# Performance work log

Hardware: AMD Instinct MI355X
Metric: run time of the kernel (lower is better)

Reference implementation:

```python
import jax, jax.numpy as jnp
import numpy as np
import math

PHI = (1.0 + math.sqrt(5.0)) / 2.0
ALPHA = 0.01
I_ROT = math.pi / 2.0
B, IN, H = 4096, 1024, 1024
GIN = IN + 4 * H  # input + 2H (h flat) + 2H (surfaced flat)


def _mag(z):
    return jnp.sqrt(z[..., 0] ** 2 + z[..., 1] ** 2 + 1e-8)


def _phase(z):
    return jnp.arctan2(z[..., 1], z[..., 0] + 1e-10)


@jax.custom_vjp
def fractal_compress(mag):
    m = jnp.maximum(mag, 1e-8)
    return m ** (2.0 / 3.0)


def _fc_fwd(mag):
    m = jnp.maximum(mag, 1e-8)
    c = m ** (2.0 / 3.0)
    return c, c / (m + 1e-6)


def _fc_bwd(ratio, g):
    return (g * jnp.minimum(ratio, 2.0),)


fractal_compress.defvjp(_fc_fwd, _fc_bwd)


def converge(z):
    mag = _mag(z)
    ph = _phase(z)
    cm = fractal_compress(mag)
    return jnp.stack([cm * jnp.cos(ph), cm * jnp.sin(ph)], axis=-1)


def resonance_gate(a, b):
    d = _phase(a) - _phase(b)
    return jnp.cos(d / 2.0) ** 2


def _uni(k, shape, fan_in):
    s = (1.0 / PHI) / math.sqrt(fan_in)
    return jax.random.uniform(k, shape, jnp.float32, -s, s)


def setup_inputs() -> dict:
    key = jax.random.key(0)
    ks = jax.random.split(key, 12)
    return {
        "x_t": jax.random.normal(ks[0], (B, IN), jnp.float32),
        "h_prev": jax.random.normal(ks[1], (B, H, 2), jnp.float32),
        "c_prev": jax.random.normal(ks[2], (B, H, 2), jnp.float32),
        "d_prev": jax.random.normal(ks[3], (B, H, 2), jnp.float32),
        "b_prev": jax.random.uniform(ks[4], (B, 1), jnp.float32),
        "Wf_w": _uni(ks[5], (H, GIN), GIN), "Wf_b": jnp.zeros((H,), jnp.float32),
        "Wi_w": _uni(ks[6], (H, GIN), GIN), "Wi_b": jnp.zeros((H,), jnp.float32),
        "Wo_w": _uni(ks[7], (H, GIN), GIN), "Wo_b": jnp.zeros((H,), jnp.float32),
        "Wc_w": _uni(ks[8], (2 * H, GIN), GIN), "Wc_b": jnp.zeros((2 * H,), jnp.float32),
        "Wr_w": _uni(ks[9], (2 * H, IN), IN), "Wr_b": jnp.zeros((2 * H,), jnp.float32),
        "theta": jnp.full((H,), I_ROT, jnp.float32),
    }


def reference(x_t, h_prev, c_prev, d_prev, b_prev,
              Wf_w, Wf_b, Wi_w, Wi_b, Wo_w, Wo_b, Wc_w, Wc_b, Wr_w, Wr_b, theta):
    batch = x_t.shape[0]
    hid = theta.shape[0]

    # boundary: real input -> complex
    x_complex = (x_t @ Wr_w.T + Wr_b).reshape(batch, hid, 2)

    # memory surfacing from the (detached) worldline
    d_read = jax.lax.stop_gradient(d_prev)
    T = resonance_gate(x_complex, d_read)                      # (B, H)
    d_mag = _mag(d_read)[..., None]                            # (B, H, 1)
    d_normed = d_read / (d_mag + 1e-8)
    d_scale = jnp.sqrt(jnp.clip(d_mag, 1e-6, 20.0))
    surfaced = d_normed * d_scale * T[..., None]               # (B, H, 2)

    combined = jnp.concatenate(
        [x_t, h_prev.reshape(batch, -1), surfaced.reshape(batch, -1)], axis=-1)

    f_raw = combined @ Wf_w.T + Wf_b
    i_raw = combined @ Wi_w.T + Wi_b
    o_raw = combined @ Wo_w.T + Wo_b

    temperature = (2.0 * b_prev + 1e-4)[..., None]             # (B, 1, 1)
    gate_stack = jnp.stack([f_raw, i_raw, o_raw], axis=-1)     # (B, H, 3)
    gw = jax.nn.softmax(gate_stack / temperature, axis=-1)
    f_t, i_t, o_t = gw[..., 0], gw[..., 1], gw[..., 2]

    g_raw = combined @ Wc_w.T + Wc_b
    g_t = jnp.stack([jnp.tanh(g_raw[:, :hid]), jnp.tanh(g_raw[:, hid:])], axis=-1)

    # convergence: released surface -> fractal-compressed -> worldline
    released = (1.0 - f_t)[..., None] * c_prev
    compressed = jnp.clip(converge(released), -10.0, 10.0)
    d_t = jax.lax.stop_gradient(d_prev) + ALPHA * compressed
    d_mag_new = _mag(d_t)[..., None]
    d_t = jnp.where(d_mag_new > 20.0, d_t * (20.0 / d_mag_new), d_t)

    # cell update + i-rotation
    c_updated = f_t[..., None] * c_prev + i_t[..., None] * g_t
    cos_t = jnp.cos(theta)[None, :, None]
    sin_t = jnp.sin(theta)[None, :, None]
    cr, ci = c_updated[..., 0:1], c_updated[..., 1:2]
    c_t = jnp.concatenate([cos_t * cr - sin_t * ci, sin_t * cr + cos_t * ci], axis=-1)

    c_squashed = jnp.stack([jnp.tanh(c_t[..., 0]), jnp.tanh(c_t[..., 1])], axis=-1)
    h_raw = o_t[..., None] * c_squashed
    G = resonance_gate(h_raw, d_t)
    h_t = G[..., None] * h_raw

    # balance update from energy split
    conv_e = (_mag(released) ** 2).sum(axis=-1, keepdims=True)
    emer_e = (_mag(h_t) ** 2).sum(axis=-1, keepdims=True)
    b_measured = conv_e / (conv_e + emer_e + 1e-8)
    b_t = 0.99 * b_prev + 0.01 * b_measured

    h_t = jnp.nan_to_num(h_t, nan=0.0)
    c_t = jnp.nan_to_num(c_t, nan=0.0)
    d_t = jnp.nan_to_num(d_t, nan=0.0)
    b_t = jnp.nan_to_num(b_t, nan=0.5)
    return (h_t, c_t, d_t, b_t)
```

## Files before the change

### kernel.cpp

```cpp
#include <hip/hip_runtime.h>
#include <math.h>

typedef unsigned short u16;
typedef unsigned int u32;
typedef u16 u16x4 __attribute__((ext_vector_type(4)));
typedef float f32x2 __attribute__((ext_vector_type(2)));
typedef float f32x4 __attribute__((ext_vector_type(4)));
typedef __bf16 bf16x8 __attribute__((ext_vector_type(8)));

__device__ __forceinline__ u16 f2bf(float f){
  u32 u = __builtin_bit_cast(u32, f);
  u32 r = u + 0x7FFFu + ((u >> 16) & 1u);
  return (u16)(r >> 16);
}
__device__ __forceinline__ float bf2f(u16 h){
  u32 u = ((u32)h) << 16;
  return __builtin_bit_cast(float, u);
}
__device__ __forceinline__ float ftanh(float x){
  float e = __expf(2.f*x);
  return 1.f - 2.f/(e+1.f);
}

typedef __attribute__((address_space(1))) const unsigned int gas_u32;
typedef __attribute__((address_space(3))) unsigned int las_u32;
__device__ __forceinline__ void gload_lds16(const void* g, void* l){
  __builtin_amdgcn_global_load_lds((gas_u32*)g, (las_u32*)l, 16, 0, 0);
}

__global__ __launch_bounds__(256) void cvt_hi(const float* __restrict__ in, u16* __restrict__ out, int n4){
  int i = blockIdx.x*256 + threadIdx.x;
  if (i >= n4) return;
  f32x4 v = *(const f32x4*)(in + (size_t)i*4);
  u16x4 o;
  #pragma unroll
  for (int j=0;j<4;++j) o[j]=f2bf(v[j]);
  *(u16x4*)(out + (size_t)i*4) = o;
}

__global__ __launch_bounds__(256) void cvt_hilo(const float* __restrict__ in, u16* __restrict__ hi, u16* __restrict__ lo, int n4){
  int i = blockIdx.x*256 + threadIdx.x;
  if (i >= n4) return;
  f32x4 v = *(const f32x4*)(in + (size_t)i*4);
  u16x4 oh, ol;
  #pragma unroll
  for (int j=0;j<4;++j){ u16 h=f2bf(v[j]); oh[j]=h; ol[j]=f2bf(v[j]-bf2f(h)); }
  *(u16x4*)(hi + (size_t)i*4) = oh;
  *(u16x4*)(lo + (size_t)i*4) = ol;
}

__global__ __launch_bounds__(256) void cvt_xh(const float* __restrict__ x, const float* __restrict__ h,
                                              u16* __restrict__ cA, u16* __restrict__ xlo){
  int b = blockIdx.y;
  int c0 = (blockIdx.x*256 + threadIdx.x)*4;
  f32x4 v;
  if (c0 < 1024) v = *(const f32x4*)(x + (size_t)b*1024 + c0);
  else           v = *(const f32x4*)(h + (size_t)b*2048 + (c0-1024));
  u16x4 hi4;
  #pragma unroll
  for (int j=0;j<4;++j) hi4[j]=f2bf(v[j]);
  *(u16x4*)(cA + (size_t)b*5120 + c0) = hi4;
  if (c0 < 1024){
    u16x4 lo4;
    #pragma unroll
    for (int j=0;j<4;++j) lo4[j]=f2bf(v[j]-bf2f(hi4[j]));
    *(u16x4*)(xlo + (size_t)b*1024 + c0) = lo4;
  }
}

__global__ __launch_bounds__(256) void prep_surf(const float* __restrict__ xc, const float* __restrict__ dp,
                                                 const int* __restrict__ smap, float* __restrict__ Scmp,
                                                 u16* __restrict__ cA, int cap){
  int i = blockIdx.x*256 + threadIdx.x;
  int b = i >> 10, h = i & 1023;
  f32x2 z = *(const f32x2*)(xc + 2*(size_t)i);
  f32x2 d = *(const f32x2*)(dp + 2*(size_t)i);
  float zx = z[0] + 1e-10f, dx = d[0] + 1e-10f;
  float hz = sqrtf(zx*zx + z[1]*z[1]);
  float hd = sqrtf(dx*dx + d[1]*d[1]);
  float cosd = (zx*dx + z[1]*d[1]) / fmaxf(hz*hd, 1e-30f);
  float T = 0.5f + 0.5f*cosd;
  float dmag = sqrtf(d[0]*d[0] + d[1]*d[1] + 1e-8f);
  float dscale = sqrtf(fminf(fmaxf(dmag, 1e-6f), 20.0f));
  float s = T * dscale / (dmag + 1e-8f);
  float o0 = d[0]*s, o1 = d[1]*s;
  u32 pk = (u32)f2bf(o0) | ((u32)f2bf(o1) << 16);
  *(u32*)&cA[(size_t)b*5120 + 3072 + 2*h] = pk;
  int p = smap[b];
  if (p >= 0 && p < cap)
    *(f32x2*)(Scmp + ((size_t)p*1024 + h)*2) = f32x2{o0, o1};
}

__global__ __launch_bounds__(256) void flag_rows(const float* __restrict__ bp, int* __restrict__ out,
                                                 int* __restrict__ smap, int cap){
  __shared__ int cnt;
  if (threadIdx.x==0) cnt=0;
  __syncthreads();
  for (int i=threadIdx.x; i<4096; i+=256){
    int p = -1;
    if (bp[i] < 0.04f){
      p = atomicAdd(&cnt,1);
      if (p < cap) out[1+p]=i;
    }
    smap[i] = p;
  }
  __syncthreads();
  if (threadIdx.x==0) out[0] = min(cnt, cap);
}

__global__ __launch_bounds__(256) void fix_init(const int* __restrict__ smap, const int* __restrict__ cr,
    const float* __restrict__ b0, const float* __restrict__ b1, const float* __restrict__ b2,
    float* __restrict__ C){
  int b = blockIdx.x;
  int p = smap[b];
  if (p < 0 || p >= cr[0]) return;
  #pragma unroll
  for (int j0=0; j0<3072; j0+=256){
    int j = j0 + threadIdx.x;
    float bb = (j<1024) ? b0[j] : ((j<2048) ? b1[j-1024] : b2[j-2048]);
    C[(size_t)b*3072 + j] = bb;
  }
}

#define LDA8(BUF,H,MH,J) (*(const bf16x8*)(sAc + ((BUF)*2+(H))*16384 + abase + (MH)*4096 + (J)*1024))
#define LDB8(BUF,H,N)    (*(const bf16x8*)(sBc + ((BUF)*2+(H))*BHTB + bbase + (N)*1024))
#define STG_A8(BUF,H,TT) { const u16* s_ = Ah + aS + (size_t)(TT)*64 + (H)*32; \
    gload_lds16(s_, dA + ((BUF)*2+(H))*8192); \
    gload_lds16(s_ + aS2, dA + ((BUF)*2+(H))*8192 + 4096); }
#define STG_B8(BUF,H,TT) { const u16* s_ = Bh + bS + (size_t)(TT)*64 + (H)*32; \
    gload_lds16(s_, dB + ((BUF)*2+(H))*(BHTB/2)); \
    if constexpr (NR==4){ gload_lds16(s_ + bS2, dB + ((BUF)*2+(H))*(BHTB/2) + 4096); } }
#define PH8(BUF,H,MH,RB,STG,DOW) do{ \
    bf16x8 af0 = LDA8(BUF,H,MH,0), af1 = LDA8(BUF,H,MH,1), af2 = LDA8(BUF,H,MH,2), af3 = LDA8(BUF,H,MH,3); \
    if (RB){ _Pragma("unroll") for(int n_=0;n_<NR;++n_) bfr[n_] = LDB8(BUF,H,n_); } \
    STG; \
    asm volatile("" ::: "memory"); \
    __builtin_amdgcn_s_barrier(); \
    asm volatile("s_waitcnt lgkmcnt(0)" ::: "memory"); \
    __builtin_amdgcn_sched_barrier(0); \
    __builtin_amdgcn_s_setprio(1); \
    _Pragma("unroll") for(int n_=0;n_<NR;++n_){ \
      acc[(MH)*4+0][n_] = __builtin_amdgcn_mfma_f32_16x16x32_bf16(af0, bfr[n_], acc[(MH)*4+0][n_],0,0,0); \
      acc[(MH)*4+1][n_] = __builtin_amdgcn_mfma_f32_16x16x32_bf16(af1, bfr[n_], acc[(MH)*4+1][n_],0,0,0); \
      acc[(MH)*4+2][n_] = __builtin_amdgcn_mfma_f32_16x16x32_bf16(af2, bfr[n_], acc[(MH)*4+2][n_],0,0,0); \
      acc[(MH)*4+3][n_] = __builtin_amdgcn_mfma_f32_16x16x32_bf16(af3, bfr[n_], acc[(MH)*4+3][n_],0,0,0); } \
    __builtin_amdgcn_s_setprio(0); \
    if (DOW) { asm volatile("s_waitcnt vmcnt(%0)" :: "i"(VN) : "memory"); } \
    asm volatile("" ::: "memory"); \
    __builtin_amdgcn_s_barrier(); \
    __builtin_amdgcn_sched_barrier(0); \
  }while(0)

template<int NR, bool OUTBF, int NB>
__global__ __launch_bounds__(512) void gemm8p(
    const u16* __restrict__ Ah, int lda,
    const u16* __restrict__ Bh, int ldb,
    const float* __restrict__ bias0, const float* __restrict__ bias1, const float* __restrict__ bias2,
    float* __restrict__ Cf, u16* __restrict__ Cb, int ldc, int K)
{
  constexpr int BN   = NR*64;
  constexpr int BHTB = BN*64;
  constexpr int VN   = (NR==4) ? 4 : 3;
  __shared__ u16 sA[4*8192];
  __shared__ u16 sB[4*(NR*2048)];
  const char* sAc = (const char*)sA;
  const char* sBc = (const char*)sB;

  const int tid = threadIdx.x, lane = tid&63, w8 = tid>>6;
  const int wr = w8>>2, wc = w8&3;
  const int l16 = lane&15;

  const int gx = gridDim.x, nwg = gx*gridDim.y;
  const int lin = blockIdx.y*gx + blockIdx.x;
  const int sw = (lin&7)*(nwg>>3) + (lin>>3);
  const int m0 = (sw / gx)*256, n0 = (sw % gx)*BN;

  const int rowS  = tid>>2;
  const int ksS   = (tid&3) ^ ((tid>>3)&3);
  const size_t aS = (size_t)(m0 + rowS)*lda + ksS*8;
  const size_t aS2= (size_t)128*lda;
  const size_t bS = (size_t)(n0 + rowS)*ldb + ksS*8;
  const size_t bS2= (size_t)128*ldb;
  u16* dA = sA + w8*512;
  u16* dB = sB + w8*512;

  const int aslot = (lane>>4) ^ ((l16>>1)&3);
  const int abase = (wr*128 + l16)*64 + aslot*16;
  const int bbase = (wc*(NR*16) + l16)*64 + aslot*16;

  f32x4 acc[8][NR];
  #pragma unroll
  for (int a=0;a<8;++a)
    #pragma unroll
    for (int b=0;b<NR;++b) acc[a][b] = f32x4{0.f,0.f,0.f,0.f};
  bf16x8 bfr[NR];

  const int NT = K>>6, NITER = K>>7;

  STG_A8(0,0,0) STG_B8(0,0,0) STG_A8(0,1,0) STG_B8(0,1,0) STG_A8(1,0,1) STG_B8(1,0,1)
  asm volatile("s_waitcnt vmcnt(%0)" :: "i"(VN) : "memory");
  asm volatile("" ::: "memory");
  __builtin_amdgcn_s_barrier();
  __builtin_amdgcn_sched_barrier(0);

  for (int i=0; i<NITER; ++i){
    const int t1 = 2*i+1;
    const int ta = min(2*i+2, NT-1);
    const int tb = min(2*i+3, NT-1);
    PH8(0,0,0,true,  STG_A8(1,1,t1), false);
    PH8(0,0,1,false, STG_B8(1,1,t1), false);
    PH8(0,1,0,true,  STG_A8(0,0,ta), false);
    PH8(0,1,1,false, STG_B8(0,0,ta), true);
    PH8(1,0,0,true,  STG_A8(0,1,ta), false);
    PH8(1,0,1,false, STG_B8(0,1,ta), false);
    PH8(1,1,0,true,  STG_A8(1,0,tb), false);
    PH8(1,1,1,false, STG_B8(1,0,tb), true);
  }
  asm volatile("s_waitcnt vmcnt(0)" ::: "memory");

  #pragma unroll
  for (int mf=0; mf<8; ++mf){
    int grow = m0 + wr*128 + mf*16 + (lane>>4)*4;
    #pragma unroll
    for (int n=0; n<NR; ++n){
      int gcol = n0 + wc*(NR*16) + n*16 + l16;
      float bb;
      if constexpr(NB==3) bb = (gcol<1024) ? bias0[gcol] : ((gcol<2048) ? bias1[gcol-1024] : bias2[gcol-2048]);
      else bb = bias0[gcol];
      #pragma unroll
      for (int r2=0;r2<4;++r2){
        float v = acc[mf][n][r2] + bb;
        if constexpr(OUTBF) Cb[(size_t)(grow+r2)*ldc + gcol] = f2bf(v);
        else                Cf[(size_t)(grow+r2)*ldc + gcol] = v;
      }
    }
  }
}

#define STG128(USRC, BW) do{ int u_=(USRC)<NT?(USRC):NT-1; \
    { const u16* s_=Ah+aS+(size_t)u_*32; gload_lds16(s_, sA+(BW)*4096+ldsb); } \
    { const u16* s_=Bh+bS+(size_t)u_*32; gload_lds16(s_, sB+(BW)*8192+ldsb); \
      gload_lds16(s_+bS2, sB+(BW)*8192+4096+ldsb); } \
    if constexpr(SPLIT){ \
      const u16* s2_=Al+aSl+(size_t)u_*32; gload_lds16(s2_, sAl+(BW)*4096+ldsb); \
      const u16* s3_=Bl+bS+(size_t)u_*32;  gload_lds16(s3_, sBl+(BW)*8192+ldsb); \
      gload_lds16(s3_+bS2, sBl+(BW)*8192+4096+ldsb); } \
  }while(0)

template<bool SPLIT, bool OUTBF>
__global__ __launch_bounds__(512) void gemm128(
    const u16* __restrict__ Ah, int lda,
    const u16* __restrict__ Al, int ldal,
    const u16* __restrict__ Bh, int ldb,
    const u16* __restrict__ Bl,
    const float* __restrict__ bias0,
    float* __restrict__ Cf, u16* __restrict__ Cb, int ldc, int K)
{
  constexpr int VN = SPLIT ? 6 : 3;
  __shared__ u16 sA [3*4096];
  __shared__ u16 sB [3*8192];
  __shared__ u16 sAl[SPLIT?3*4096:8];
  __shared__ u16 sBl[SPLIT?3*8192:8];

  const int tid=threadIdx.x, lane=tid&63, w8=tid>>6;
  const int wr=w8>>2, wc=w8&3, l16=lane&15;

  const int gx=gridDim.x, nwg=gx*gridDim.y;
  const int lin=blockIdx.y*gx+blockIdx.x;
  const int sw=(lin&7)*(nwg>>3)+(lin>>3);
  const int m0=(sw/gx)*128, n0=(sw%gx)*256;

  const int rowS=tid>>2;
  const int ksS=(tid&3)^((tid>>3)&3);
  const size_t aS =(size_t)(m0+rowS)*lda  + ksS*8;
  const size_t aSl=(size_t)(m0+rowS)*(size_t)ldal + ksS*8;
  const size_t bS =(size_t)(n0+rowS)*ldb  + ksS*8;
  const size_t bS2=(size_t)128*ldb;
  const int ldsb = w8*512;

  const int aslot=(lane>>4)^((l16>>1)&3);
  const int abase=(wr*64+l16)*64 + aslot*16;
  const int bbase=(wc*64+l16)*64 + aslot*16;

  f32x4 acc[4][4];
  #pragma unroll
  for (int a=0;a<4;++a)
    #pragma unroll
    for (int b=0;b<4;++b) acc[a][b] = f32x4{0.f,0.f,0.f,0.f};

  const int NT = K>>5;

  STG128(0,0); STG128(1,1);
  asm volatile("s_waitcnt vmcnt(%0)" :: "i"(VN) : "memory");
  asm volatile("" ::: "memory");
  __builtin_amdgcn_s_barrier();
  __builtin_amdgcn_sched_barrier(0);

  int bufR = 0;
  for (int t=0; t<NT; ++t){
    int bufW = bufR+2; if (bufW>=3) bufW-=3;
    const char* sAc=(const char*)sA  + bufR*8192;
    const char* sBc=(const char*)sB  + bufR*16384;
    const char* sAlc=(const char*)sAl + bufR*8192;
    const char* sBlc=(const char*)sBl + bufR*16384;
    bf16x8 af[4], bf[4], afl[4], bfl[4];
    #pragma unroll
    for (int f=0; f<4; ++f){
      af[f] = *(const bf16x8*)(sAc + abase + f*1024);
      bf[f] = *(const bf16x8*)(sBc + bbase + f*1024);
      if constexpr(SPLIT){
        afl[f] = *(const bf16x8*)(sAlc + abase + f*1024);
        bfl[f] = *(const bf16x8*)(sBlc + bbase + f*1024);
      }
    }
    STG128(t+2, bufW);
    asm volatile("" ::: "memory");
    __builtin_amdgcn_s_barrier();
    asm volatile("s_waitcnt lgkmcnt(0)" ::: "memory");
    __builtin_amdgcn_sched_barrier(0);
    __builtin_amdgcn_s_setprio(1);
    #pragma unroll
    for (int mf=0; mf<4; ++mf){
      #pragma unroll
      for (int nf=0; nf<4; ++nf){
        acc[mf][nf] = __builtin_amdgcn_mfma_f32_16x16x32_bf16(af[mf], bf[nf], acc[mf][nf],0,0,0);
        if constexpr(SPLIT){
          acc[mf][nf] = __builtin_amdgcn_mfma_f32_16x16x32_bf16(afl[mf], bf[nf],  acc[mf][nf],0,0,0);
          acc[mf][nf] = __builtin_amdgcn_mfma_f32_16x16x32_bf16(af[mf],  bfl[nf], acc[mf][nf],0,0,0);
        }
      }
    }
    __builtin_amdgcn_s_setprio(0);
    asm volatile("s_waitcnt vmcnt(%0)" :: "i"(VN) : "memory");
    asm volatile("" ::: "memory");
    __builtin_amdgcn_s_barrier();
    __builtin_amdgcn_sched_barrier(0);
    bufR = (bufR==2) ? 0 : bufR+1;
  }
  asm volatile("s_waitcnt vmcnt(0)" ::: "memory");

  #pragma unroll
  for (int mf=0; mf<4; ++mf){
    int grow = m0 + wr*64 + mf*16 + (lane>>4)*4;
    #pragma unroll
    for (int nf=0; nf<4; ++nf){
      int gcol = n0 + wc*64 + nf*16 + l16;
      float bb = bias0[gcol];
      #pragma unroll
      for (int r2=0;r2<4;++r2){
        float v = acc[mf][nf][r2] + bb;
        if constexpr(OUTBF) Cb[(size_t)(grow+r2)*ldc + gcol] = f2bf(v);
        else                Cf[(size_t)(grow+r2)*ldc + gcol] = v;
      }
    }
  }
}

#define LSTR 40
#define FIX_KC 16
#define FIX_KLEN 320
__global__ __launch_bounds__(256) void gemm_fix_sk(
    const float* __restrict__ Xs, const float* __restrict__ Hs,
    const float* __restrict__ Scmp, const int* __restrict__ smap,
    const float* __restrict__ W0, const float* __restrict__ W1, const float* __restrict__ W2,
    const int* __restrict__ cr, float* __restrict__ C)
{
  const int count = cr[0];
  const int m0 = blockIdx.y * 128;
  if (m0 >= count) return;
  const int* rows = cr + 1;
  const int kbeg = blockIdx.z * FIX_KLEN;
  const int kend = kbeg + FIX_KLEN;

  __shared__ u16 sAh[128*LSTR];
  __shared__ u16 sAl[128*LSTR];
  __shared__ u16 sBh[128*LSTR];
  __shared__ u16 sBl[128*LSTR];

  const int tid = threadIdx.x;
  const int n0 = blockIdx.x * 128;
  int seg = n0 >> 10;
  const float* W = (seg==0) ? W0 : (seg==1 ? W1 : W2);
  int nw = n0 & 1023;

  const int wave = tid >> 6, lane = tid & 63;
  const int wm = wave >> 1, wn = wave & 1;
  const int l16 = lane & 15, lk8 = (lane >> 4) * 8;

  f32x4 acc[4][4];
  #pragma unroll
  for (int a=0;a<4;++a)
    #pragma unroll
    for (int b=0;b<4;++b) acc[a][b] = f32x4{0.f,0.f,0.f,0.f};

  for (int k0 = kbeg; k0 < kend; k0 += 32){
    #pragma unroll
    for (int i=0;i<4;++i){
      int flat = tid + i*256;
      int r  = flat >> 3;
      int c4 = flat & 7;
      int kk = k0 + c4*4;
      int mrow = rows[min(m0 + r, count-1)];
      const float* srcA;
      if (kk < 1024)      srcA = Xs + (size_t)mrow*1024 + kk;
      else if (kk < 3072) srcA = Hs + (size_t)mrow*2048 + (kk - 1024);
      else                srcA = Scmp + (size_t)smap[mrow]*2048 + (kk - 3072);
      f32x4 va = *(const f32x4*)srcA;
      f32x4 vb = *(const f32x4*)(W + (size_t)(nw + r)*5120 + kk);
      u16x4 ah, bh, al, bl;
      #pragma unroll
      for (int j=0;j<4;++j){
        u16 hA = f2bf(va[j]); ah[j] = hA; al[j] = f2bf(va[j] - bf2f(hA));
        u16 hB = f2bf(vb[j]); bh[j] = hB; bl[j] = f2bf(vb[j] - bf2f(hB));
      }
      int o = r*LSTR + c4*4;
      *(u16x4*)&sAh[o] = ah;
      *(u16x4*)&sBh[o] = bh;
      *(u16x4*)&sAl[o] = al;
      *(u16x4*)&sBl[o] = bl;
    }
    __syncthreads();
    bf16x8 fah[4], fbh[4], fal[4], fbl[4];
    #pragma unroll
    for (int f=0; f<4; ++f){
      int ra  = (wm*64 + f*16 + l16)*LSTR + lk8;
      int rb2 = (wn*64 + f*16 + l16)*LSTR + lk8;
      fah[f] = *(const bf16x8*)&sAh[ra];
      fbh[f] = *(const bf16x8*)&sBh[rb2];
      fal[f] = *(const bf16x8*)&sAl[ra];
      fbl[f] = *(const bf16x8*)&sBl[rb2];
    }
    #pragma unroll
    for (int fm=0; fm<4; ++fm){
      #pragma unroll
      for (int fn=0; fn<4; ++fn){
        acc[fm][fn] = __builtin_amdgcn_mfma_f32_16x16x32_bf16(fah[fm], fbh[fn], acc[fm][fn], 0,0,0);
        acc[fm][fn] = __builtin_amdgcn_mfma_f32_16x16x32_bf16(fal[fm], fbh[fn], acc[fm][fn], 0,0,0);
        acc[fm][fn] = __builtin_amdgcn_mfma_f32_16x16x32_bf16(fah[fm], fbl[fn], acc[fm][fn], 0,0,0);
      }
    }
    __syncthreads();
  }

  #pragma unroll
  for (int fm=0; fm<4; ++fm){
    int trow = wm*64 + fm*16 + (lane>>4)*4;
    #pragma unroll
    for (int fn=0; fn<4; ++fn){
      int lcol = wn*64 + fn*16 + l16;
      #pragma unroll
      for (int r2=0;r2<4;++r2){
        int mi = m0 + trow + r2;
        if (mi < count){
          int mrow = rows[mi];
          atomicAdd(&C[(size_t)mrow*3072 + (n0 + lcol)], acc[fm][fn][r2]);
        }
      }
    }
  }
}

__global__ __launch_bounds__(256) void epilogue(
    const float* __restrict__ rawfio, const u16* __restrict__ rawg,
    const float* __restrict__ c_prev, const float* __restrict__ d_prev,
    const float* __restrict__ b_prev, const float* __restrict__ theta,
    float* __restrict__ out)
{
  const int b = blockIdx.x;
  const int tid = threadIdx.x;
  float* Hout = out;
  float* Cout = out + (size_t)8388608;
  float* Dout = out + (size_t)16777216;
  float* Bout = out + (size_t)25165824;
  const float bp = b_prev[b];
  const float inv_t = 1.0f / (2.0f*bp + 1e-4f);
  float conv_acc = 0.f, emer_acc = 0.f;
  const size_t rb3 = (size_t)b*3072;
  const size_t rg = (size_t)b*2048;

  #pragma unroll
  for (int j=0;j<4;++j){
    int h = tid + j*256;
    float fr = rawfio[rb3 + h];
    float ir = rawfio[rb3 + 1024 + h];
    float og = rawfio[rb3 + 2048 + h];
    float g0 = bf2f(rawg[rg + h]);
    float g1 = bf2f(rawg[rg + 1024 + h]);

    float mx = fmaxf(fr, fmaxf(ir, og));
    float ef = __expf((fr-mx)*inv_t);
    float ei = __expf((ir-mx)*inv_t);
    float eo = __expf((og-mx)*inv_t);
    float inv_s = 1.0f/(ef+ei+eo);
    float ft = ef*inv_s, it = ei*inv_s, ot = eo*inv_s;

    f32x2 cp = *(const f32x2*)(c_prev + 2*((size_t)b*1024 + h));
    f32x2 dp = *(const f32x2*)(d_prev + 2*((size_t)b*1024 + h));

    float r0 = (1.f-ft)*cp[0], r1 = (1.f-ft)*cp[1];
    float rm2 = r0*r0 + r1*r1;
    conv_acc += rm2 + 1e-8f;
    float rmag = sqrtf(rm2 + 1e-8f);
    float cm = __expf(0.66666667f * __logf(rmag));
    float rx = r0 + 1e-10f;
    float hr = fmaxf(sqrtf(rx*rx + r1*r1), 1e-30f);
    float invhr = cm / hr;
    float comp0 = fminf(fmaxf(rx*invhr, -10.f), 10.f);
    float comp1 = fminf(fmaxf(r1*invhr, -10.f), 10.f);

    float d0 = dp[0] + 0.01f*comp0;
    float d1 = dp[1] + 0.01f*comp1;
    float dmn = sqrtf(d0*d0 + d1*d1 + 1e-8f);
    if (dmn > 20.f){ float sc = 20.f/dmn; d0*=sc; d1*=sc; }

    float gt0 = ftanh(g0), gt1 = ftanh(g1);
    float cu0 = ft*cp[0] + it*gt0;
    float cu1 = ft*cp[1] + it*gt1;
    float th = theta[h];
    float sth, cth;
    __sincosf(th, &sth, &cth);
    float c0 = cth*cu0 - sth*cu1;
    float c1 = sth*cu0 + cth*cu1;
    float cs0 = ftanh(c0), cs1 = ftanh(c1);
    float hr0 = ot*cs0, hr1 = ot*cs1;

    float hx = hr0 + 1e-10f, dx = d0 + 1e-10f;
    float hh = sqrtf(hx*hx + hr1*hr1);
    float hd = sqrtf(dx*dx + d1*d1);
    float cosd = (hx*dx + hr1*d1) / fmaxf(hh*hd, 1e-30f);
    float G = 0.5f + 0.5f*cosd;
    float h0 = G*hr0, h1 = G*hr1;
    emer_acc += h0*h0 + h1*h1 + 1e-8f;

    h0 = (h0==h0)?h0:0.f;  h1 = (h1==h1)?h1:0.f;
    c0 = (c0==c0)?c0:0.f;  c1 = (c1==c1)?c1:0.f;
    d0 = (d0==d0)?d0:0.f;  d1 = (d1==d1)?d1:0.f;

    size_t oi = 2*((size_t)b*1024 + h);
    *(f32x2*)(Hout+oi) = f32x2{h0,h1};
    *(f32x2*)(Cout+oi) = f32x2{c0,c1};
    *(f32x2*)(Dout+oi) = f32x2{d0,d1};
  }

  #pragma unroll
  for (int off=32; off; off>>=1){
    conv_acc += __shfl_down(conv_acc, off);
    emer_acc += __shfl_down(emer_acc, off);
  }
  __shared__ float sred[8];
  int wv = tid>>6, ln = tid&63;
  if (ln==0){ sred[wv]=conv_acc; sred[4+wv]=emer_acc; }
  __syncthreads();
  if (tid==0){
    float cv = sred[0]+sred[1]+sred[2]+sred[3];
    float em = sred[4]+sred[5]+sred[6]+sred[7];
    float bm = cv/(cv+em+1e-8f);
    float bt = 0.99f*bp + 0.01f*bm;
    bt = (bt==bt)?bt:0.5f;
    Bout[b] = bt;
  }
}

extern "C" void kernel_launch(void* const* d_in, const int* in_sizes, int n_in,
                              void* d_out, int out_size, void* d_ws, size_t ws_size,
                              hipStream_t stream)
{
  const float* x_t    = (const float*)d_in[0];
  const float* h_prev = (const float*)d_in[1];
  const float* c_prev = (const float*)d_in[2];
  const float* d_prev = (const float*)d_in[3];
  const float* b_prev = (const float*)d_in[4];
  const float* Wf_w   = (const float*)d_in[5];
  const float* Wf_b   = (const float*)d_in[6];
  const float* Wi_w   = (const float*)d_in[7];
  const float* Wi_b   = (const float*)d_in[8];
  const float* Wo_w   = (const float*)d_in[9];
  const float* Wo_b   = (const float*)d_in[10];
  const float* Wc_w   = (const float*)d_in[11];
  const float* Wc_b   = (const float*)d_in[12];
  const float* Wr_w   = (const float*)d_in[13];
  const float* Wr_b   = (const float*)d_in[14];
  const float* theta  = (const float*)d_in[15];

  char* W = (char*)d_ws;
  float* rawfio = (float*)W;
  float* xc     = (float*)W;
  u16*   Wr_hi  = (u16*)(W + 50331648);
  u16*   Wr_lo  = (u16*)(W + 50331648 + 4194304);
  u16*   x_lo   = (u16*)(W + 50331648 + 8388608);
  u16*   raw_g  = (u16*)(W + 50331648);
  u16*   cA     = (u16*)(W + 67108864);
  u16*   WD     = (u16*)(W + 109051904);
  int*   idx    = (int*)(W + 140509184);
  int*   smap   = (int*)(W + 140509184 + 16388);
  float* Scmp   = (float*)(W + 140546048);
  long long avail = (long long)ws_size - 140546048LL;
  int cap = (int)(avail > 0 ? avail / 8192 : 0);
  if (cap > 1024) cap = 1024;

  dim3 blk(256);

  cvt_xh<<<dim3(3,4096), blk, 0, stream>>>(x_t, h_prev, cA, x_lo);
  cvt_hilo<<<2048, blk, 0, stream>>>(Wr_w, Wr_hi, Wr_lo, 524288);
  gemm128<true,false><<<dim3(8,32), dim3(512), 0, stream>>>(
      cA, 5120, x_lo, 1024, Wr_hi, 1024, Wr_lo,
      Wr_b, xc, nullptr, 2048, 1024);
  flag_rows<<<1, blk, 0, stream>>>(b_prev, idx, smap, cap);
  prep_surf<<<16384, blk, 0, stream>>>(xc, d_prev, smap, Scmp, cA, cap);
  cvt_hi<<<5120, blk, 0, stream>>>(Wf_w, WD, 1310720);
  cvt_hi<<<5120, blk, 0, stream>>>(Wi_w, WD + (size_t)1024*5120, 1310720);
  cvt_hi<<<5120, blk, 0, stream>>>(Wo_w, WD + (size_t)2048*5120, 1310720);
  gemm8p<4,false,3><<<dim3(12,16), dim3(512), 0, stream>>>(
      cA, 5120, WD, 5120, Wf_b, Wi_b, Wo_b, rawfio, nullptr, 3072, 5120);
  fix_init<<<4096, blk, 0, stream>>>(smap, idx, Wf_b, Wi_b, Wo_b, rawfio);
  gemm_fix_sk<<<dim3(24,8,FIX_KC), blk, 0, stream>>>(
      x_t, h_prev, Scmp, smap, Wf_w, Wi_w, Wo_w, idx, rawfio);
  cvt_hi<<<10240, blk, 0, stream>>>(Wc_w, WD, 2621440);
  gemm128<false,true><<<dim3(8,32), dim3(512), 0, stream>>>(
      cA, 5120, nullptr, 0, WD, 5120, nullptr,
      Wc_b, nullptr, raw_g, 2048, 5120);
  epilogue<<<4096, blk, 0, stream>>>(rawfio, raw_g, c_prev, d_prev, b_prev, theta, (float*)d_out);
}
```

Baseline: 525.4 us.

## Fuse prep kernels, decouple fix-up GEMM output, deepen gemm128 pipeline

Merges the x/h conversion, Wr hi/lo split, rawfix zeroing and row flagging into one prep0 launch, and the three weight conversions into one cvtW3 launch. The fix-up GEMM now accumulates into a separate compact rawfix buffer indexed by flagged-row position. The epilogue adds the biases and selects that buffer for flagged rows, which removes fix_init and the ordering dependency on gemm8p. The Wc gemm128 uses five LDS stages instead of three for deeper prefetch, and gemm8p waits on loads more often. This trades more LDS per block (lower occupancy risk) and a fixed cap of 256 flagged rows for fewer launches and better overlap.

```diff
diff --git a/kernel.cpp b/kernel.cpp
--- a/kernel.cpp
+++ b/kernel.cpp
@@ -8,6 +8,8 @@
 typedef float f32x4 __attribute__((ext_vector_type(4)));
 typedef __bf16 bf16x8 __attribute__((ext_vector_type(8)));
 
+#define CAPF 256
+
 __device__ __forceinline__ u16 f2bf(float f){
   u32 u = __builtin_bit_cast(u32, f);
   u32 r = u + 0x7FFFu + ((u >> 16) & 1u);
@@ -26,6 +28,73 @@
 typedef __attribute__((address_space(3))) unsigned int las_u32;
 __device__ __forceinline__ void gload_lds16(const void* g, void* l){
   __builtin_amdgcn_global_load_lds((gas_u32*)g, (las_u32*)l, 16, 0, 0);
+}
+
+__global__ __launch_bounds__(256) void prep0(
+    const float* __restrict__ x, const float* __restrict__ h,
+    u16* __restrict__ cA, u16* __restrict__ xlo,
+    const float* __restrict__ Wr, u16* __restrict__ Wr_hi, u16* __restrict__ Wr_lo,
+    const float* __restrict__ bp, int* __restrict__ idx, int* __restrict__ smap,
+    float* __restrict__ rawfix)
+{
+  const int bx = blockIdx.x, tid = threadIdx.x;
+  if (bx < 12288){
+    int b = bx / 3, cb = bx - b*3;
+    int c0 = (cb*256 + tid)*4;
+    f32x4 v;
+    if (c0 < 1024) v = *(const f32x4*)(x + (size_t)b*1024 + c0);
+    else           v = *(const f32x4*)(h + (size_t)b*2048 + (c0-1024));
+    u16x4 hi4;
+    #pragma unroll
+    for (int j=0;j<4;++j) hi4[j]=f2bf(v[j]);
+    *(u16x4*)(cA + (size_t)b*5120 + c0) = hi4;
+    if (c0 < 1024){
+      u16x4 lo4;
+      #pragma unroll
+      for (int j=0;j<4;++j) lo4[j]=f2bf(v[j]-bf2f(hi4[j]));
+      *(u16x4*)(xlo + (size_t)b*1024 + c0) = lo4;
+    }
+  } else if (bx < 14336){
+    int i = (bx-12288)*256 + tid;
+    f32x4 v = *(const f32x4*)(Wr + (size_t)i*4);
+    u16x4 oh, ol;
+    #pragma unroll
+    for (int j=0;j<4;++j){ u16 hh=f2bf(v[j]); oh[j]=hh; ol[j]=f2bf(v[j]-bf2f(hh)); }
+    *(u16x4*)(Wr_hi + (size_t)i*4) = oh;
+    *(u16x4*)(Wr_lo + (size_t)i*4) = ol;
+  } else if (bx < 15104){
+    int i = (bx-14336)*256 + tid;
+    *(f32x4*)(rawfix + (size_t)i*4) = f32x4{0.f,0.f,0.f,0.f};
+  } else {
+    __shared__ int cnt;
+    if (tid==0) cnt=0;
+    __syncthreads();
+    for (int i=tid; i<4096; i+=256){
+      int p = -1;
+      if (bp[i] < 0.04f){
+        p = atomicAdd(&cnt,1);
+        if (p < CAPF) idx[1+p]=i;
+      }
+      smap[i] = p;
+    }
+    __syncthreads();
+    if (tid==0) idx[0] = min(cnt, CAPF);
+  }
+}
+
+__global__ __launch_bounds__(256) void cvtW3(
+    const float* __restrict__ W0, const float* __restrict__ W1, const float* __restrict__ W2,
+    u16* __restrict__ out)
+{
+  int i = blockIdx.x*256 + threadIdx.x;
+  int seg = i / 1310720;
+  int w = i - seg*1310720;
+  const float* src = (seg==0) ? W0 : (seg==1 ? W1 : W2);
+  f32x4 v = *(const f32x4*)(src + (size_t)w*4);
+  u16x4 o;
+  #pragma unroll
+  for (int j=0;j<4;++j) o[j]=f2bf(v[j]);
+  *(u16x4*)(out + (size_t)seg*5242880 + (size_t)w*4) = o;
 }
 
 __global__ __launch_bounds__(256) void cvt_hi(const float* __restrict__ in, u16* __restrict__ out, int n4){
@@ -38,39 +107,9 @@
   *(u16x4*)(out + (size_t)i*4) = o;
 }
 
-__global__ __launch_bounds__(256) void cvt_hilo(const float* __restrict__ in, u16* __restrict__ hi, u16* __restrict__ lo, int n4){
-  int i = blockIdx.x*256 + threadIdx.x;
-  if (i >= n4) return;
-  f32x4 v = *(const f32x4*)(in + (size_t)i*4);
-  u16x4 oh, ol;
-  #pragma unroll
-  for (int j=0;j<4;++j){ u16 h=f2bf(v[j]); oh[j]=h; ol[j]=f2bf(v[j]-bf2f(h)); }
-  *(u16x4*)(hi + (size_t)i*4) = oh;
-  *(u16x4*)(lo + (size_t)i*4) = ol;
-}
-
-__global__ __launch_bounds__(256) void cvt_xh(const float* __restrict__ x, const float* __restrict__ h,
-                                              u16* __restrict__ cA, u16* __restrict__ xlo){
-  int b = blockIdx.y;
-  int c0 = (blockIdx.x*256 + threadIdx.x)*4;
-  f32x4 v;
-  if (c0 < 1024) v = *(const f32x4*)(x + (size_t)b*1024 + c0);
-  else           v = *(const f32x4*)(h + (size_t)b*2048 + (c0-1024));
-  u16x4 hi4;
-  #pragma unroll
-  for (int j=0;j<4;++j) hi4[j]=f2bf(v[j]);
-  *(u16x4*)(cA + (size_t)b*5120 + c0) = hi4;
-  if (c0 < 1024){
-    u16x4 lo4;
-    #pragma unroll
-    for (int j=0;j<4;++j) lo4[j]=f2bf(v[j]-bf2f(hi4[j]));
-    *(u16x4*)(xlo + (size_t)b*1024 + c0) = lo4;
-  }
-}
-
 __global__ __launch_bounds__(256) void prep_surf(const float* __restrict__ xc, const float* __restrict__ dp,
                                                  const int* __restrict__ smap, float* __restrict__ Scmp,
-                                                 u16* __restrict__ cA, int cap){
+                                                 u16* __restrict__ cA){
   int i = blockIdx.x*256 + threadIdx.x;
   int b = i >> 10, h = i & 1023;
   f32x2 z = *(const f32x2*)(xc + 2*(size_t)i);
@@ -87,39 +126,8 @@
   u32 pk = (u32)f2bf(o0) | ((u32)f2bf(o1) << 16);
   *(u32*)&cA[(size_t)b*5120 + 3072 + 2*h] = pk;
   int p = smap[b];
-  if (p >= 0 && p < cap)
+  if (p >= 0 && p < CAPF)
     *(f32x2*)(Scmp + ((size_t)p*1024 + h)*2) = f32x2{o0, o1};
-}
-
-__global__ __launch_bounds__(256) void flag_rows(const float* __restrict__ bp, int* __restrict__ out,
-                                                 int* __restrict__ smap, int cap){
-  __shared__ int cnt;
-  if (threadIdx.x==0) cnt=0;
-  __syncthreads();
-  for (int i=threadIdx.x; i<4096; i+=256){
-    int p = -1;
-    if (bp[i] < 0.04f){
-      p = atomicAdd(&cnt,1);
-      if (p < cap) out[1+p]=i;
-    }
-    smap[i] = p;
-  }
-  __syncthreads();
-  if (threadIdx.x==0) out[0] = min(cnt, cap);
-}
-
-__global__ __launch_bounds__(256) void fix_init(const int* __restrict__ smap, const int* __restrict__ cr,
-    const float* __restrict__ b0, const float* __restrict__ b1, const float* __restrict__ b2,
-    float* __restrict__ C){
-  int b = blockIdx.x;
-  int p = smap[b];
-  if (p < 0 || p >= cr[0]) return;
-  #pragma unroll
-  for (int j0=0; j0<3072; j0+=256){
-    int j = j0 + threadIdx.x;
-    float bb = (j<1024) ? b0[j] : ((j<2048) ? b1[j-1024] : b2[j-2048]);
-    C[(size_t)b*3072 + j] = bb;
-  }
 }
 
 #define LDA8(BUF,H,MH,J) (*(const bf16x8*)(sAc + ((BUF)*2+(H))*16384 + abase + (MH)*4096 + (J)*1024))
@@ -129,7 +137,7 @@
     gload_lds16(s_ + aS2, dA + ((BUF)*2+(H))*8192 + 4096); }
 #define STG_B8(BUF,H,TT) { const u16* s_ = Bh + bS + (size_t)(TT)*64 + (H)*32; \
     gload_lds16(s_, dB + ((BUF)*2+(H))*(BHTB/2)); \
-    if constexpr (NR==4){ gload_lds16(s_ + bS2, dB + ((BUF)*2+(H))*(BHTB/2) + 4096); } }
+    gload_lds16(s_ + bS2, dB + ((BUF)*2+(H))*(BHTB/2) + 4096); }
 #define PH8(BUF,H,MH,RB,STG,DOW) do{ \
     bf16x8 af0 = LDA8(BUF,H,MH,0), af1 = LDA8(BUF,H,MH,1), af2 = LDA8(BUF,H,MH,2), af3 = LDA8(BUF,H,MH,3); \
     if (RB){ _Pragma("unroll") for(int n_=0;n_<NR;++n_) bfr[n_] = LDB8(BUF,H,n_); } \
@@ -160,7 +168,7 @@
 {
   constexpr int BN   = NR*64;
   constexpr int BHTB = BN*64;
-  constexpr int VN   = (NR==4) ? 4 : 3;
+  constexpr int VN   = 8;
   __shared__ u16 sA[4*8192];
   __shared__ u16 sB[4*(NR*2048)];
   const char* sAc = (const char*)sA;
@@ -208,11 +216,11 @@
     const int ta = min(2*i+2, NT-1);
     const int tb = min(2*i+3, NT-1);
     PH8(0,0,0,true,  STG_A8(1,1,t1), false);
-    PH8(0,0,1,false, STG_B8(1,1,t1), false);
+    PH8(0,0,1,false, STG_B8(1,1,t1), true);
     PH8(0,1,0,true,  STG_A8(0,0,ta), false);
     PH8(0,1,1,false, STG_B8(0,0,ta), true);
     PH8(1,0,0,true,  STG_A8(0,1,ta), false);
-    PH8(1,0,1,false, STG_B8(0,1,ta), false);
+    PH8(1,0,1,false, STG_B8(0,1,ta), true);
     PH8(1,1,0,true,  STG_A8(1,0,tb), false);
     PH8(1,1,1,false, STG_B8(1,0,tb), true);
   }
@@ -247,7 +255,7 @@
       gload_lds16(s3_+bS2, sBl+(BW)*8192+4096+ldsb); } \
   }while(0)
 
-template<bool SPLIT, bool OUTBF>
+template<bool SPLIT, bool OUTBF, int BUFS>
 __global__ __launch_bounds__(512) void gemm128(
     const u16* __restrict__ Ah, int lda,
     const u16* __restrict__ Al, int ldal,
@@ -256,11 +264,13 @@
     const float* __restrict__ bias0,
     float* __restrict__ Cf, u16* __restrict__ Cb, int ldc, int K)
 {
-  constexpr int VN = SPLIT ? 6 : 3;
-  __shared__ u16 sA [3*4096];
-  __shared__ u16 sB [3*8192];
-  __shared__ u16 sAl[SPLIT?3*4096:8];
-  __shared__ u16 sBl[SPLIT?3*8192:8];
+  constexpr int LPS = SPLIT ? 6 : 3;
+  constexpr int VN  = (BUFS-2)*LPS;
+  constexpr int PRE = BUFS-1;
+  __shared__ u16 sA [BUFS*4096];
+  __shared__ u16 sB [BUFS*8192];
+  __shared__ u16 sAl[SPLIT?BUFS*4096:8];
+  __shared__ u16 sBl[SPLIT?BUFS*8192:8];
 
   const int tid=threadIdx.x, lane=tid&63, w8=tid>>6;
   const int wr=w8>>2, wc=w8&3, l16=lane&15;
@@ -290,7 +300,8 @@
 
   const int NT = K>>5;
 
-  STG128(0,0); STG128(1,1);
+  #pragma unroll
+  for (int u=0; u<PRE; ++u){ STG128(u,u); }
   asm volatile("s_waitcnt vmcnt(%0)" :: "i"(VN) : "memory");
   asm volatile("" ::: "memory");
   __builtin_amdgcn_s_barrier();
@@ -298,7 +309,7 @@
 
   int bufR = 0;
   for (int t=0; t<NT; ++t){
-    int bufW = bufR+2; if (bufW>=3) bufW-=3;
+    int bufW = (bufR==0) ? BUFS-1 : bufR-1;
     const char* sAc=(const char*)sA  + bufR*8192;
     const char* sBc=(const char*)sB  + bufR*16384;
     const char* sAlc=(const char*)sAl + bufR*8192;
@@ -313,7 +324,7 @@
         bfl[f] = *(const bf16x8*)(sBlc + bbase + f*1024);
       }
     }
-    STG128(t+2, bufW);
+    STG128(t+PRE, bufW);
     asm volatile("" ::: "memory");
     __builtin_amdgcn_s_barrier();
     asm volatile("s_waitcnt lgkmcnt(0)" ::: "memory");
@@ -335,7 +346,7 @@
     asm volatile("" ::: "memory");
     __builtin_amdgcn_s_barrier();
     __builtin_amdgcn_sched_barrier(0);
-    bufR = (bufR==2) ? 0 : bufR+1;
+    bufR = (bufR+1==BUFS) ? 0 : bufR+1;
   }
   asm volatile("s_waitcnt vmcnt(0)" ::: "memory");
 
@@ -363,7 +374,7 @@
     const float* __restrict__ Xs, const float* __restrict__ Hs,
     const float* __restrict__ Scmp, const int* __restrict__ smap,
     const float* __restrict__ W0, const float* __restrict__ W1, const float* __restrict__ W2,
-    const int* __restrict__ cr, float* __restrict__ C)
+    const int* __restrict__ cr, float* __restrict__ Cfix)
 {
   const int count = cr[0];
   const int m0 = blockIdx.y * 128;
@@ -400,7 +411,8 @@
       int r  = flat >> 3;
       int c4 = flat & 7;
       int kk = k0 + c4*4;
-      int mrow = rows[min(m0 + r, count-1)];
+      int mi = min(m0 + r, count-1);
+      int mrow = rows[mi];
       const float* srcA;
       if (kk < 1024)      srcA = Xs + (size_t)mrow*1024 + kk;
       else if (kk < 3072) srcA = Hs + (size_t)mrow*2048 + (kk - 1024);
@@ -452,8 +464,7 @@
       for (int r2=0;r2<4;++r2){
         int mi = m0 + trow + r2;
         if (mi < count){
-          int mrow = rows[mi];
-          atomicAdd(&C[(size_t)mrow*3072 + (n0 + lcol)], acc[fm][fn][r2]);
+          atomicAdd(&Cfix[(size_t)mi*3072 + (n0 + lcol)], acc[fm][fn][r2]);
         }
       }
     }
@@ -462,6 +473,8 @@
 
 __global__ __launch_bounds__(256) void epilogue(
     const float* __restrict__ rawfio, const u16* __restrict__ rawg,
+    const float* __restrict__ rawfix, const int* __restrict__ smap, const int* __restrict__ cr,
+    const float* __restrict__ bf0, const float* __restrict__ bf1, const float* __restrict__ bf2,
     const float* __restrict__ c_prev, const float* __restrict__ d_prev,
     const float* __restrict__ b_prev, const float* __restrict__ theta,
     float* __restrict__ out)
@@ -477,13 +490,23 @@
   float conv_acc = 0.f, emer_acc = 0.f;
   const size_t rb3 = (size_t)b*3072;
   const size_t rg = (size_t)b*2048;
+  const int p = smap[b];
+  const bool fx = (p >= 0 && p < cr[0]);
+  const size_t rfx = (size_t)p*3072;
 
   #pragma unroll
   for (int j=0;j<4;++j){
     int h = tid + j*256;
-    float fr = rawfio[rb3 + h];
-    float ir = rawfio[rb3 + 1024 + h];
-    float og = rawfio[rb3 + 2048 + h];
+    float fr, ir, og;
+    if (fx){
+      fr = rawfix[rfx + h]        + bf0[h];
+      ir = rawfix[rfx + 1024 + h] + bf1[h];
+      og = rawfix[rfx + 2048 + h] + bf2[h];
+    } else {
+      fr = rawfio[rb3 + h];
+      ir = rawfio[rb3 + 1024 + h];
+      og = rawfio[rb3 + 2048 + h];
+    }
     float g0 = bf2f(rawg[rg + h]);
     float g1 = bf2f(rawg[rg + 1024 + h]);
 
@@ -594,30 +617,26 @@
   int*   idx    = (int*)(W + 140509184);
   int*   smap   = (int*)(W + 140509184 + 16388);
   float* Scmp   = (float*)(W + 140546048);
-  long long avail = (long long)ws_size - 140546048LL;
-  int cap = (int)(avail > 0 ? avail / 8192 : 0);
-  if (cap > 1024) cap = 1024;
+  float* rawfix = (float*)(W + 140546048 + (size_t)CAPF*2048*4);
 
   dim3 blk(256);
 
-  cvt_xh<<<dim3(3,4096), blk, 0, stream>>>(x_t, h_prev, cA, x_lo);
-  cvt_hilo<<<2048, blk, 0, stream>>>(Wr_w, Wr_hi, Wr_lo, 524288);
-  gemm128<true,false><<<dim3(8,32), dim3(512), 0, stream>>>(
+  prep0<<<15105, blk, 0, stream>>>(x_t, h_prev, cA, x_lo, Wr_w, Wr_hi, Wr_lo,
+                                   b_prev, idx, smap, rawfix);
+  gemm128<true,false,3><<<dim3(8,32), dim3(512), 0, stream>>>(
       cA, 5120, x_lo, 1024, Wr_hi, 1024, Wr_lo,
       Wr_b, xc, nullptr, 2048, 1024);
-  flag_rows<<<1, blk, 0, stream>>>(b_prev, idx, smap, cap);
-  prep_surf<<<16384, blk, 0, stream>>>(xc, d_prev, smap, Scmp, cA, cap);
-  cvt_hi<<<5120, blk, 0, stream>>>(Wf_w, WD, 1310720);
-  cvt_hi<<<5120, blk, 0, stream>>>(Wi_w, WD + (size_t)1024*5120, 1310720);
-  cvt_hi<<<5120, blk, 0, stream>>>(Wo_w, WD + (size_t)2048*5120, 1310720);
+  prep_surf<<<16384, blk, 0, stream>>>(xc, d_prev, smap, Scmp, cA);
+  gemm_fix_sk<<<dim3(24,8,FIX_KC), blk, 0, stream>>>(
+      x_t, h_prev, Scmp, smap, Wf_w, Wi_w, Wo_w, idx, rawfix);
+  cvtW3<<<15360, blk, 0, stream>>>(Wf_w, Wi_w, Wo_w, WD);
   gemm8p<4,false,3><<<dim3(12,16), dim3(512), 0, stream>>>(
       cA, 5120, WD, 5120, Wf_b, Wi_b, Wo_b, rawfio, nullptr, 3072, 5120);
-  fix_init<<<4096, blk, 0, stream>>>(smap, idx, Wf_b, Wi_b, Wo_b, rawfio);
-  gemm_fix_sk<<<dim3(24,8,FIX_KC), blk, 0, stream>>>(
-      x_t, h_prev, Scmp, smap, Wf_w, Wi_w, Wo_w, idx, rawfio);
   cvt_hi<<<10240, blk, 0, stream>>>(Wc_w, WD, 2621440);
-  gemm128<false,true><<<dim3(8,32), dim3(512), 0, stream>>>(
+  gemm128<false,true,5><<<dim3(8,32), dim3(512), 0, stream>>>(
       cA, 5120, nullptr, 0, WD, 5120, nullptr,
       Wc_b, nullptr, raw_g, 2048, 5120);
-  epilogue<<<4096, blk, 0, stream>>>(rawfio, raw_g, c_prev, d_prev, b_prev, theta, (float*)d_out);
-}
+  epilogue<<<4096, blk, 0, stream>>>(rawfio, raw_g, rawfix, smap, idx,
+                                     Wf_b, Wi_b, Wo_b,
+                                     c_prev, d_prev, b_prev, theta, (float*)d_out);
+}
```

New measurement: 497.8 us. -5.3%, faster.
